# Performance work log

Hardware: AMD Instinct MI355X
Metric: run time of the kernel (lower is better)

The kernel has to match this reference:

```python
import jax, jax.numpy as jnp
import numpy as np

N = 50000   # nodes
E = 800000  # edges (avg degree 16)
H = 4       # heads
IN = 256    # input feature dim
HID = 64    # hidden dim per head (H*HID = 256 = layer-1 indim)
CLS = 40    # num classes


def setup_inputs():
    key = jax.random.key(0)
    ks = jax.random.split(key, 32)
    s = 0.05  # small init scale keeps exp(leaky_relu(...)) numerically tame
    rn = lambda i, shape: jax.random.normal(ks[i], shape, jnp.float32) * s
    inp = {
        'features': jax.random.normal(ks[0], (N, IN), jnp.float32),
        'src': jax.random.randint(ks[1], (E,), 0, N, jnp.int32),
        'dst': jax.random.randint(ks[2], (E,), 0, N, jnp.int32),
        # layer 0 (per-head stacked): fc, attn_l, attn_r
        'W0': rn(3, (H, IN, HID)), 'b0': rn(4, (H, HID)),
        'al0': rn(5, (H, HID)), 'alb0': rn(6, (H,)),
        'ar0': rn(7, (H, HID)), 'arb0': rn(8, (H,)),
        # layer 1 (indim = H*HID = 256), with residual fc per head
        'W1': rn(9, (H, H * HID, HID)), 'b1': rn(10, (H, HID)),
        'al1': rn(11, (H, HID)), 'alb1': rn(12, (H,)),
        'ar1': rn(13, (H, HID)), 'arb1': rn(14, (H,)),
        'R1': rn(15, (H, H * HID, HID)), 'Rb1': rn(16, (H, HID)),
        # final layer (single head, indim = H*HID, outdim = CLS), residual fc
        'Wf': rn(17, (H * HID, CLS)), 'bf': rn(18, (CLS,)),
        'alf': rn(19, (CLS,)), 'alfb': rn(20, (1,)),
        'arf': rn(21, (CLS,)), 'arfb': rn(22, (1,)),
        'Rf': rn(23, (H * HID, CLS)), 'Rbf': rn(24, (CLS,)),
    }
    return inp


def _head(x, W, b, al, alb, ar, arb, src, dst):
    # GATPrepare: ft = Linear(x); a1 = attn_l(ft); a2 = attn_r(ft)
    ft = x @ W + b                              # [N, D]
    a1 = ft @ al + alb                          # [N]
    a2 = ft @ ar + arb                          # [N]
    # edge phase 1: attention = exp(leaky_relu(a2[src] + a1[dst]))
    e = jnp.exp(jax.nn.leaky_relu(a2[src] + a1[dst], 0.01))      # [E]
    # a_sum pass: segment-sum of attention at dst, then normalize (edge softmax)
    denom = jax.ops.segment_sum(e, dst, num_segments=N)          # [N]
    att = (e / denom[dst])[:, None]                              # [E, 1]
    # src_mul_edge + sum: scatter-sum ft[src] * attention into dst
    return jax.ops.segment_sum(ft[src] * att, dst, num_segments=N)  # [N, D]


def reference(features, src, dst,
              W0, b0, al0, alb0, ar0, arb0,
              W1, b1, al1, alb1, ar1, arb1, R1, Rb1,
              Wf, bf, alf, alfb, arf, arfb, Rf, Rbf):
    # layer 0: no residual (hardcoded residual=False for first layer)
    heads = [jax.nn.elu(_head(features, W0[h], b0[h], al0[h], alb0[h], ar0[h], arb0[h], src, dst))
             for h in range(H)]
    x = jnp.concatenate(heads, axis=1)          # [N, H*HID]
    # layer 1: residual via residual_fc (indim != hiddendim)
    heads = [jax.nn.elu(x @ R1[h] + Rb1[h]
                        + _head(x, W1[h], b1[h], al1[h], alb1[h], ar1[h], arb1[h], src, dst))
             for h in range(H)]
    x = jnp.concatenate(heads, axis=1)          # [N, H*HID]
    # final layer: single head to num_classes, residual via residual_fc
    out = jax.nn.elu(x @ Rf + Rbf + _head(x, Wf, bf, alf, alfb, arf, arfb, src, dst))
    return out                                   # [N, CLS]
```

## Files before the change

kernel.cpp:

```cpp
#include <hip/hip_runtime.h>
#include <hip/hip_bf16.h>
#include <math.h>

#define NN   50000
#define NE   800000
#define NHEAD 4
#define HIDD 64
#define DD   256
#define NCLS 40

typedef __attribute__((ext_vector_type(8))) short s8v;
typedef __attribute__((ext_vector_type(4))) float f4v;

static __device__ __forceinline__ float elu_f(float x) {
  return x > 0.f ? x : expm1f(x);
}
static __device__ __forceinline__ float lrelu_exp(float x) {
  float v = x > 0.f ? x : 0.01f * x;
  return expf(v);
}
static __device__ __forceinline__ unsigned short f2bf(float x) {
  union { float f; unsigned u; } v; v.f = x;
  unsigned r = v.u + 0x7fffu + ((v.u >> 16) & 1u);
  return (unsigned short)(r >> 16);
}
static __device__ __forceinline__ float bf2f(unsigned short b) {
  union { unsigned u; float f; } v; v.u = ((unsigned)b) << 16;
  return v.f;
}
static __device__ __forceinline__ float rdlanef(float v, int l) {
  return __uint_as_float(__builtin_amdgcn_readlane(__float_as_uint(v), l));
}

__global__ void pack_w_bf(const float* __restrict__ W,
                          unsigned short* __restrict__ Bh,
                          unsigned short* __restrict__ Bl) {
  int i = blockIdx.x * 256 + threadIdx.x;
  if (i >= 65536) return;
  int n = i >> 8, k = i & 255;
  float v = W[(n >> 6) * (256 * 64) + k * 64 + (n & 63)];
  unsigned short hi = f2bf(v);
  Bh[i] = hi;
  Bl[i] = f2bf(v - bf2f(hi));
}

__global__ void pack_wf_bf(const float* __restrict__ Wf,
                           unsigned short* __restrict__ Bh,
                           unsigned short* __restrict__ Bl) {
  int i = blockIdx.x * 256 + threadIdx.x;
  if (i >= 64 * 256) return;
  int n = i >> 8, k = i & 255;
  float v = (n < NCLS) ? Wf[k * NCLS + n] : 0.f;
  unsigned short hi = f2bf(v);
  Bh[i] = hi;
  Bl[i] = f2bf(v - bf2f(hi));
}

__global__ void split_bf(const float* __restrict__ A,
                         unsigned short* __restrict__ Ah,
                         unsigned short* __restrict__ Al, int n4) {
  int i = blockIdx.x * 256 + threadIdx.x;
  if (i >= n4) return;
  float4 v = ((const float4*)A)[i];
  ushort4 h, l;
  h.x = f2bf(v.x); l.x = f2bf(v.x - bf2f(h.x));
  h.y = f2bf(v.y); l.y = f2bf(v.y - bf2f(h.y));
  h.z = f2bf(v.z); l.z = f2bf(v.z - bf2f(h.z));
  h.w = f2bf(v.w); l.w = f2bf(v.w - bf2f(h.w));
  ((ushort4*)Ah)[i] = h;
  ((ushort4*)Al)[i] = l;
}

template <int BN, int OBF>
__global__ __launch_bounds__(256) void gemm_bf16x3(
    const unsigned short* __restrict__ Ah, const unsigned short* __restrict__ Al,
    const unsigned short* __restrict__ Bth, const unsigned short* __restrict__ Btl,
    const float* __restrict__ bias, float* __restrict__ C,
    unsigned short* __restrict__ Cb,
    int M, int Nc) {
  constexpr int K = 256;
  constexpr int RS = 40;
  constexpr int WM = (BN == 128) ? 2 : 4;
  constexpr int WN = 4 / WM;
  constexpr int MI = (128 / WM) / 16;
  constexpr int NI = (BN / WN) / 16;

  __shared__ unsigned short sAh[128 * RS];
  __shared__ unsigned short sAl[128 * RS];
  __shared__ unsigned short sBh[BN * RS];
  __shared__ unsigned short sBl[BN * RS];

  const int tid = threadIdx.x;
  const int lane = tid & 63;
  const int w = tid >> 6;
  const int wr = w / WN, wc = w % WN;
  const int rowbase = wr * (128 / WM);
  const int colbase = wc * (BN / WN);
  const int row0 = blockIdx.x * 128;
  const int col0 = blockIdx.y * BN;
  const int lm = lane & 15;
  const int lk8 = (lane >> 4) * 8;

  f4v acc[MI][NI];
#pragma unroll
  for (int i = 0; i < MI; i++)
#pragma unroll
    for (int j = 0; j < NI; j++) acc[i][j] = (f4v)(0.f);

  for (int k0 = 0; k0 < K; k0 += 32) {
    __syncthreads();
#pragma unroll
    for (int i = 0; i < 2; ++i) {
      int idx = tid + i * 256;
      int r = idx >> 2, seg = idx & 3;
      int grow = row0 + r;
      s8v hv = (s8v)(short)0, lv = (s8v)(short)0;
      if (grow < M) {
        size_t g = (size_t)grow * K + k0 + seg * 8;
        hv = *(const s8v*)(Ah + g);
        lv = *(const s8v*)(Al + g);
      }
      *(s8v*)&sAh[r * RS + seg * 8] = hv;
      *(s8v*)&sAl[r * RS + seg * 8] = lv;
    }
#pragma unroll
    for (int i = 0; i < BN / 64; ++i) {
      int idx = tid + i * 256;
      int n = idx >> 2, seg = idx & 3;
      size_t g = (size_t)(col0 + n) * K + k0 + seg * 8;
      *(s8v*)&sBh[n * RS + seg * 8] = *(const s8v*)(Bth + g);
      *(s8v*)&sBl[n * RS + seg * 8] = *(const s8v*)(Btl + g);
    }
    __syncthreads();

    s8v ah[MI], al_[MI], bh[NI], bl_[NI];
#pragma unroll
    for (int mi = 0; mi < MI; ++mi) {
      int base = (rowbase + mi * 16 + lm) * RS + lk8;
      ah[mi] = *(const s8v*)&sAh[base];
      al_[mi] = *(const s8v*)&sAl[base];
    }
#pragma unroll
    for (int ni = 0; ni < NI; ++ni) {
      int base = (colbase + ni * 16 + lm) * RS + lk8;
      bh[ni] = *(const s8v*)&sBh[base];
      bl_[ni] = *(const s8v*)&sBl[base];
    }
#pragma unroll
    for (int mi = 0; mi < MI; ++mi)
#pragma unroll
      for (int ni = 0; ni < NI; ++ni)
        acc[mi][ni] = __builtin_amdgcn_mfma_f32_16x16x32_bf16(ah[mi], bh[ni], acc[mi][ni], 0, 0, 0);
#pragma unroll
    for (int mi = 0; mi < MI; ++mi)
#pragma unroll
      for (int ni = 0; ni < NI; ++ni)
        acc[mi][ni] = __builtin_amdgcn_mfma_f32_16x16x32_bf16(ah[mi], bl_[ni], acc[mi][ni], 0, 0, 0);
#pragma unroll
    for (int mi = 0; mi < MI; ++mi)
#pragma unroll
      for (int ni = 0; ni < NI; ++ni)
        acc[mi][ni] = __builtin_amdgcn_mfma_f32_16x16x32_bf16(al_[mi], bh[ni], acc[mi][ni], 0, 0, 0);
  }

#pragma unroll
  for (int ni = 0; ni < NI; ++ni) {
    int col = col0 + colbase + ni * 16 + lm;
    if (col >= Nc) continue;
    float bv = bias[col];
#pragma unroll
    for (int mi = 0; mi < MI; ++mi) {
      int rbase = row0 + rowbase + mi * 16 + (lane >> 4) * 4;
#pragma unroll
      for (int r = 0; r < 4; ++r) {
        int row = rbase + r;
        if (row < M) {
          float o = acc[mi][ni][r] + bv;
          if (OBF) Cb[(size_t)row * Nc + col] = f2bf(o);
          else     C[(size_t)row * Nc + col] = o;
        }
      }
    }
  }
}

__global__ void attn_scores4_bf(const unsigned short* __restrict__ ftb,
                                const float* __restrict__ al, const float* __restrict__ alb,
                                const float* __restrict__ ar, const float* __restrict__ arb,
                                float* __restrict__ a1, float* __restrict__ a2, int n_nodes) {
  int n = blockIdx.x * 4 + (threadIdx.x >> 6);
  if (n >= n_nodes) return;
  int lane = threadIdx.x & 63;
  ushort4 fb = *(const ushort4*)(ftb + (size_t)n * 256 + lane * 4);
  float4 f = make_float4(bf2f(fb.x), bf2f(fb.y), bf2f(fb.z), bf2f(fb.w));
  float4 l4 = *(const float4*)(al + lane * 4);
  float4 r4 = *(const float4*)(ar + lane * 4);
  float p1 = f.x * l4.x + f.y * l4.y + f.z * l4.z + f.w * l4.w;
  float p2 = f.x * r4.x + f.y * r4.y + f.z * r4.z + f.w * r4.w;
#pragma unroll
  for (int m = 1; m < 16; m <<= 1) {
    p1 += __shfl_xor(p1, m);
    p2 += __shfl_xor(p2, m);
  }
  if ((lane & 15) == 0) {
    int h = lane >> 4;
    a1[n * 4 + h] = p1 + alb[h];
    a2[n * 4 + h] = p2 + arb[h];
  }
}

__global__ void attn_scores1(const float* __restrict__ ftf,
                             const float* __restrict__ alf, const float* __restrict__ alfb,
                             const float* __restrict__ arf, const float* __restrict__ arfb,
                             float* __restrict__ a1, float* __restrict__ a2, int n_nodes) {
  int n = blockIdx.x * 4 + (threadIdx.x >> 6);
  if (n >= n_nodes) return;
  int lane = threadIdx.x & 63;
  float v = (lane < NCLS) ? ftf[(size_t)n * NCLS + lane] : 0.f;
  float p1 = (lane < NCLS) ? v * alf[lane] : 0.f;
  float p2 = (lane < NCLS) ? v * arf[lane] : 0.f;
#pragma unroll
  for (int m = 1; m < 64; m <<= 1) {
    p1 += __shfl_xor(p1, m);
    p2 += __shfl_xor(p2, m);
  }
  if (lane == 0) {
    a1[n] = p1 + alfb[0];
    a2[n] = p2 + arfb[0];
  }
}

__global__ void count_deg(const int* __restrict__ dst, int* __restrict__ deg) {
  int e = blockIdx.x * blockDim.x + threadIdx.x;
  if (e < NE) atomicAdd(&deg[dst[e]], 1);
}

__global__ void scan_deg(const int* __restrict__ deg, int* __restrict__ row_ptr, int n) {
  __shared__ int partials[1024];
  int t = threadIdx.x;
  int chunk = (n + 1023) >> 10;
  int base = t * chunk;
  int lim = min(base + chunk, n);
  int sum = 0;
  for (int i = base; i < lim; ++i) sum += deg[i];
  partials[t] = sum;
  __syncthreads();
  for (int off = 1; off < 1024; off <<= 1) {
    int v = (t >= off) ? partials[t - off] : 0;
    __syncthreads();
    partials[t] += v;
    __syncthreads();
  }
  int run = (t == 0) ? 0 : partials[t - 1];
  if (t == 0) row_ptr[0] = 0;
  for (int i = base; i < lim; ++i) {
    run += deg[i];
    row_ptr[i + 1] = run;
  }
}

__global__ void copy_int(const int* __restrict__ a, int* __restrict__ b, int n) {
  int i = blockIdx.x * blockDim.x + threadIdx.x;
  if (i < n) b[i] = a[i];
}

__global__ void scatter_e(const int* __restrict__ dst, int* __restrict__ cursor,
                          int* __restrict__ eidx) {
  int e = blockIdx.x * blockDim.x + threadIdx.x;
  if (e >= NE) return;
  int d = dst[e];
  int pos = atomicAdd(&cursor[d], 1);
  eidx[pos] = e;
}

__global__ __launch_bounds__(256) void gather_wave4(
    const unsigned short* __restrict__ ftb, const float* __restrict__ a1,
    const float* __restrict__ a2, const float* __restrict__ res,
    const int* __restrict__ row_ptr, const int* __restrict__ eidx,
    const int* __restrict__ src,
    unsigned short* __restrict__ outh, unsigned short* __restrict__ outl) {
  const int n = blockIdx.x * 4 + (threadIdx.x >> 6);
  if (n >= NN) return;
  const int lane = threadIdx.x & 63;
  const int c = lane >> 4;
  const int b = row_ptr[n], en = row_ptr[n + 1];
  const int deg = en - b;
  const float4 a1v = *(const float4*)(a1 + (size_t)n * 4);
  float4 accv = make_float4(0.f, 0.f, 0.f, 0.f);
  float den = 0.f;

  for (int cb = 0; cb < deg; cb += 64) {
    int cnt = min(64, deg - cb);
    int s = 0;
    float4 wv = make_float4(0.f, 0.f, 0.f, 0.f);
    if (lane < cnt) {
      s = src[eidx[b + cb + lane]];
      float4 as_ = *(const float4*)(a2 + (size_t)s * 4);
      wv.x = lrelu_exp(as_.x + a1v.x);
      wv.y = lrelu_exp(as_.y + a1v.y);
      wv.z = lrelu_exp(as_.z + a1v.z);
      wv.w = lrelu_exp(as_.w + a1v.w);
    }
    int i = 0;
    for (; i + 4 <= cnt; i += 4) {
      int s0 = __builtin_amdgcn_readlane(s, i + 0);
      int s1 = __builtin_amdgcn_readlane(s, i + 1);
      int s2 = __builtin_amdgcn_readlane(s, i + 2);
      int s3 = __builtin_amdgcn_readlane(s, i + 3);
      ushort4 f0 = *(const ushort4*)(ftb + (size_t)s0 * DD + lane * 4);
      ushort4 f1 = *(const ushort4*)(ftb + (size_t)s1 * DD + lane * 4);
      ushort4 f2 = *(const ushort4*)(ftb + (size_t)s2 * DD + lane * 4);
      ushort4 f3 = *(const ushort4*)(ftb + (size_t)s3 * DD + lane * 4);
      float x0 = rdlanef(wv.x, i + 0), y0 = rdlanef(wv.y, i + 0),
            z0 = rdlanef(wv.z, i + 0), u0 = rdlanef(wv.w, i + 0);
      float x1 = rdlanef(wv.x, i + 1), y1 = rdlanef(wv.y, i + 1),
            z1 = rdlanef(wv.z, i + 1), u1 = rdlanef(wv.w, i + 1);
      float x2 = rdlanef(wv.x, i + 2), y2 = rdlanef(wv.y, i + 2),
            z2 = rdlanef(wv.z, i + 2), u2 = rdlanef(wv.w, i + 2);
      float x3 = rdlanef(wv.x, i + 3), y3 = rdlanef(wv.y, i + 3),
            z3 = rdlanef(wv.z, i + 3), u3 = rdlanef(wv.w, i + 3);
      float w0 = (c == 0) ? x0 : (c == 1) ? y0 : (c == 2) ? z0 : u0;
      float w1 = (c == 0) ? x1 : (c == 1) ? y1 : (c == 2) ? z1 : u1;
      float w2 = (c == 0) ? x2 : (c == 1) ? y2 : (c == 2) ? z2 : u2;
      float w3 = (c == 0) ? x3 : (c == 1) ? y3 : (c == 2) ? z3 : u3;
      accv.x = fmaf(bf2f(f0.x), w0, accv.x);
      accv.y = fmaf(bf2f(f0.y), w0, accv.y);
      accv.z = fmaf(bf2f(f0.z), w0, accv.z);
      accv.w = fmaf(bf2f(f0.w), w0, accv.w);
      accv.x = fmaf(bf2f(f1.x), w1, accv.x);
      accv.y = fmaf(bf2f(f1.y), w1, accv.y);
      accv.z = fmaf(bf2f(f1.z), w1, accv.z);
      accv.w = fmaf(bf2f(f1.w), w1, accv.w);
      accv.x = fmaf(bf2f(f2.x), w2, accv.x);
      accv.y = fmaf(bf2f(f2.y), w2, accv.y);
      accv.z = fmaf(bf2f(f2.z), w2, accv.z);
      accv.w = fmaf(bf2f(f2.w), w2, accv.w);
      accv.x = fmaf(bf2f(f3.x), w3, accv.x);
      accv.y = fmaf(bf2f(f3.y), w3, accv.y);
      accv.z = fmaf(bf2f(f3.z), w3, accv.z);
      accv.w = fmaf(bf2f(f3.w), w3, accv.w);
      den += (w0 + w1) + (w2 + w3);
    }
    for (; i < cnt; ++i) {
      int si = __builtin_amdgcn_readlane(s, i);
      float fx = rdlanef(wv.x, i), fy = rdlanef(wv.y, i),
            fz = rdlanef(wv.z, i), fw = rdlanef(wv.w, i);
      float wc = (c == 0) ? fx : (c == 1) ? fy : (c == 2) ? fz : fw;
      ushort4 fv = *(const ushort4*)(ftb + (size_t)si * DD + lane * 4);
      accv.x = fmaf(bf2f(fv.x), wc, accv.x);
      accv.y = fmaf(bf2f(fv.y), wc, accv.y);
      accv.z = fmaf(bf2f(fv.z), wc, accv.z);
      accv.w = fmaf(bf2f(fv.w), wc, accv.w);
      den += wc;
    }
  }
  float invden = (deg > 0) ? 1.f / den : 0.f;
  float4 r = (res != nullptr) ? *(const float4*)(res + (size_t)n * DD + lane * 4)
                              : make_float4(0.f, 0.f, 0.f, 0.f);
  float4 o;
  o.x = elu_f(r.x + accv.x * invden);
  o.y = elu_f(r.y + accv.y * invden);
  o.z = elu_f(r.z + accv.z * invden);
  o.w = elu_f(r.w + accv.w * invden);
  ushort4 h, l;
  h.x = f2bf(o.x); l.x = f2bf(o.x - bf2f(h.x));
  h.y = f2bf(o.y); l.y = f2bf(o.y - bf2f(h.y));
  h.z = f2bf(o.z); l.z = f2bf(o.z - bf2f(h.z));
  h.w = f2bf(o.w); l.w = f2bf(o.w - bf2f(h.w));
  *(ushort4*)(outh + (size_t)n * DD + lane * 4) = h;
  *(ushort4*)(outl + (size_t)n * DD + lane * 4) = l;
}

__global__ __launch_bounds__(64) void gather_fused1(
    const float* __restrict__ ft, const float* __restrict__ a1,
    const float* __restrict__ a2, const float* __restrict__ res,
    const int* __restrict__ row_ptr, const int* __restrict__ eidx,
    const int* __restrict__ src, float* __restrict__ out) {
  const int n = blockIdx.x;
  const int d = threadIdx.x;
  const int b = row_ptr[n], en = row_ptr[n + 1];
  const int deg = en - b;
  const float a1n = a1[n];
  float acc = 0.f;
  float den = 0.f;

  for (int cb = 0; cb < deg; cb += 64) {
    int cnt = min(64, deg - cb);
    int s = 0;
    float wv = 0.f;
    if (d < cnt) {
      s = src[eidx[b + cb + d]];
      wv = lrelu_exp(a2[s] + a1n);
    }
    int i = 0;
    for (; i + 4 <= cnt; i += 4) {
      int s0 = __builtin_amdgcn_readlane(s, i + 0);
      int s1 = __builtin_amdgcn_readlane(s, i + 1);
      int s2 = __builtin_amdgcn_readlane(s, i + 2);
      int s3 = __builtin_amdgcn_readlane(s, i + 3);
      float w0 = rdlanef(wv, i + 0), w1 = rdlanef(wv, i + 1);
      float w2 = rdlanef(wv, i + 2), w3 = rdlanef(wv, i + 3);
      if (d < NCLS) {
        float v0 = ft[(size_t)s0 * NCLS + d];
        float v1 = ft[(size_t)s1 * NCLS + d];
        float v2 = ft[(size_t)s2 * NCLS + d];
        float v3 = ft[(size_t)s3 * NCLS + d];
        acc = fmaf(v0, w0, acc);
        acc = fmaf(v1, w1, acc);
        acc = fmaf(v2, w2, acc);
        acc = fmaf(v3, w3, acc);
      }
      den += (w0 + w1) + (w2 + w3);
    }
    for (; i < cnt; ++i) {
      int si = __builtin_amdgcn_readlane(s, i);
      float wi = rdlanef(wv, i);
      if (d < NCLS) acc = fmaf(ft[(size_t)si * NCLS + d], wi, acc);
      den += wi;
    }
  }
  float invden = (deg > 0) ? 1.f / den : 0.f;
  if (d < NCLS) {
    float r = res[(size_t)n * NCLS + d];
    out[(size_t)n * NCLS + d] = elu_f(r + acc * invden);
  }
}

extern "C" void kernel_launch(void* const* d_in, const int* in_sizes, int n_in,
                              void* d_out, int out_size, void* d_ws, size_t ws_size,
                              hipStream_t stream) {
  const float* features = (const float*)d_in[0];
  const int* src = (const int*)d_in[1];
  const int* dst = (const int*)d_in[2];
  const float* W0 = (const float*)d_in[3];
  const float* b0 = (const float*)d_in[4];
  const float* al0 = (const float*)d_in[5];
  const float* alb0 = (const float*)d_in[6];
  const float* ar0 = (const float*)d_in[7];
  const float* arb0 = (const float*)d_in[8];
  const float* W1 = (const float*)d_in[9];
  const float* b1 = (const float*)d_in[10];
  const float* al1 = (const float*)d_in[11];
  const float* alb1 = (const float*)d_in[12];
  const float* ar1 = (const float*)d_in[13];
  const float* arb1 = (const float*)d_in[14];
  const float* R1 = (const float*)d_in[15];
  const float* Rb1 = (const float*)d_in[16];
  const float* Wf = (const float*)d_in[17];
  const float* bfc = (const float*)d_in[18];
  const float* alf = (const float*)d_in[19];
  const float* alfb = (const float*)d_in[20];
  const float* arf = (const float*)d_in[21];
  const float* arfb = (const float*)d_in[22];
  const float* Rf = (const float*)d_in[23];
  const float* Rbf = (const float*)d_in[24];
  float* out = (float*)d_out;

  float* p = (float*)d_ws;
  float* B1 = p;  p += (size_t)NN * 256;
  float* B2 = p;  p += (size_t)NN * 256;
  float* B3 = p;  p += (size_t)NN * 256;
  float* a1 = p;  p += (size_t)NN * 4;
  float* a2 = p;  p += (size_t)NN * 4;
  unsigned short* us = (unsigned short*)p;
  unsigned short* Wp0h = us; us += 65536;
  unsigned short* Wp0l = us; us += 65536;
  unsigned short* Wp1h = us; us += 65536;
  unsigned short* Wp1l = us; us += 65536;
  unsigned short* Rp1h = us; us += 65536;
  unsigned short* Rp1l = us; us += 65536;
  unsigned short* Wfh = us;  us += 64 * 256;
  unsigned short* Wfl = us;  us += 64 * 256;
  unsigned short* Rfh = us;  us += 64 * 256;
  unsigned short* Rfl = us;  us += 64 * 256;
  unsigned short* Ah = us;   us += (size_t)NN * 256;
  unsigned short* Al = us;   us += (size_t)NN * 256;
  unsigned short* ftb = us;  us += (size_t)NN * 256;
  int* ip = (int*)us;
  int* row_ptr = ip; ip += NN + 1;
  int* cursor = ip;  ip += NN;
  int* deg = ip;     ip += NN;
  int* eidx = ip;    ip += NE;

  const int EB = (NE + 255) / 256;
  const int N4 = NN * 64;

  pack_w_bf<<<256, 256, 0, stream>>>(W0, Wp0h, Wp0l);
  pack_w_bf<<<256, 256, 0, stream>>>(W1, Wp1h, Wp1l);
  pack_w_bf<<<256, 256, 0, stream>>>(R1, Rp1h, Rp1l);
  pack_wf_bf<<<64, 256, 0, stream>>>(Wf, Wfh, Wfl);
  pack_wf_bf<<<64, 256, 0, stream>>>(Rf, Rfh, Rfl);

  hipMemsetAsync(deg, 0, NN * sizeof(int), stream);
  count_deg<<<EB, 256, 0, stream>>>(dst, deg);
  scan_deg<<<1, 1024, 0, stream>>>(deg, row_ptr, NN);
  copy_int<<<(NN + 255) / 256, 256, 0, stream>>>(row_ptr, cursor, NN);
  scatter_e<<<EB, 256, 0, stream>>>(dst, cursor, eidx);

  const int MB = (NN + 127) / 128;
  dim3 gbig(MB, 2);
  dim3 gsm(MB, 1);
  const int GW = (NN + 3) / 4;

  split_bf<<<(N4 + 255) / 256, 256, 0, stream>>>(features, Ah, Al, N4);
  gemm_bf16x3<128, 1><<<gbig, 256, 0, stream>>>(Ah, Al, Wp0h, Wp0l, b0, nullptr, ftb, NN, 256);
  attn_scores4_bf<<<(NN + 3) / 4, 256, 0, stream>>>(ftb, al0, alb0, ar0, arb0, a1, a2, NN);
  gather_wave4<<<GW, 256, 0, stream>>>(ftb, a1, a2, nullptr, row_ptr, eidx, src, Ah, Al);

  gemm_bf16x3<128, 1><<<gbig, 256, 0, stream>>>(Ah, Al, Wp1h, Wp1l, b1, nullptr, ftb, NN, 256);
  gemm_bf16x3<128, 0><<<gbig, 256, 0, stream>>>(Ah, Al, Rp1h, Rp1l, Rb1, B3, nullptr, NN, 256);
  attn_scores4_bf<<<(NN + 3) / 4, 256, 0, stream>>>(ftb, al1, alb1, ar1, arb1, a1, a2, NN);
  gather_wave4<<<GW, 256, 0, stream>>>(ftb, a1, a2, B3, row_ptr, eidx, src, Ah, Al);

  gemm_bf16x3<64, 0><<<gsm, 256, 0, stream>>>(Ah, Al, Wfh, Wfl, bfc, B1, nullptr, NN, NCLS);
  gemm_bf16x3<64, 0><<<gsm, 256, 0, stream>>>(Ah, Al, Rfh, Rfl, Rbf, B2, nullptr, NN, NCLS);
  attn_scores1<<<(NN + 3) / 4, 256, 0, stream>>>(B1, alf, alfb, arf, arfb, a1, a2, NN);
  gather_fused1<<<NN, 64, 0, stream>>>(B1, a1, a2, B2, row_ptr, eidx, src, out);
}
```

Baseline: 734.5 us.

## Merge weight-pack launches, fold cursor init into scan, deepen gather unroll with LDS weights

Five weight-packing launches become one kernel that picks its source by block index. The scan kernel now writes the cursor array directly, which removes the copy_int launch. The 256-wide gather stores per-edge attention weights in shared memory and reads the lane's head weight from there, replacing sixteen readlanes plus select chains per four edges. Both gather kernels unroll eight edges per iteration to keep more loads in flight. The trade-offs are extra register pressure, shared-memory use, and a manual lgkmcnt wait that relies on the whole wave staying in lockstep, since no barrier is used.

```diff
diff --git a/kernel.cpp b/kernel.cpp
--- a/kernel.cpp
+++ b/kernel.cpp
@@ -32,25 +32,26 @@
   return __uint_as_float(__builtin_amdgcn_readlane(__float_as_uint(v), l));
 }
 
-__global__ void pack_w_bf(const float* __restrict__ W,
-                          unsigned short* __restrict__ Bh,
-                          unsigned short* __restrict__ Bl) {
-  int i = blockIdx.x * 256 + threadIdx.x;
-  if (i >= 65536) return;
+__global__ void pack_all(const float* __restrict__ W0, const float* __restrict__ W1,
+                         const float* __restrict__ R1, const float* __restrict__ Wf,
+                         const float* __restrict__ Rf,
+                         unsigned short* __restrict__ Wp0h, unsigned short* __restrict__ Wp0l,
+                         unsigned short* __restrict__ Wp1h, unsigned short* __restrict__ Wp1l,
+                         unsigned short* __restrict__ Rp1h, unsigned short* __restrict__ Rp1l,
+                         unsigned short* __restrict__ Wfh, unsigned short* __restrict__ Wfl,
+                         unsigned short* __restrict__ Rfh, unsigned short* __restrict__ Rfl) {
+  int bid = blockIdx.x;
+  const float* S; unsigned short *Bh, *Bl; int big;
+  if (bid < 256)      { S = W0; Bh = Wp0h; Bl = Wp0l; big = 1; }
+  else if (bid < 512) { S = W1; Bh = Wp1h; Bl = Wp1l; big = 1; bid -= 256; }
+  else if (bid < 768) { S = R1; Bh = Rp1h; Bl = Rp1l; big = 1; bid -= 512; }
+  else if (bid < 832) { S = Wf; Bh = Wfh;  Bl = Wfl;  big = 0; bid -= 768; }
+  else                { S = Rf; Bh = Rfh;  Bl = Rfl;  big = 0; bid -= 832; }
+  int i = bid * 256 + threadIdx.x;
   int n = i >> 8, k = i & 255;
-  float v = W[(n >> 6) * (256 * 64) + k * 64 + (n & 63)];
-  unsigned short hi = f2bf(v);
-  Bh[i] = hi;
-  Bl[i] = f2bf(v - bf2f(hi));
-}
-
-__global__ void pack_wf_bf(const float* __restrict__ Wf,
-                           unsigned short* __restrict__ Bh,
-                           unsigned short* __restrict__ Bl) {
-  int i = blockIdx.x * 256 + threadIdx.x;
-  if (i >= 64 * 256) return;
-  int n = i >> 8, k = i & 255;
-  float v = (n < NCLS) ? Wf[k * NCLS + n] : 0.f;
+  float v;
+  if (big) v = S[(n >> 6) * (256 * 64) + k * 64 + (n & 63)];
+  else     v = (n < NCLS) ? S[k * NCLS + n] : 0.f;
   unsigned short hi = f2bf(v);
   Bh[i] = hi;
   Bl[i] = f2bf(v - bf2f(hi));
@@ -235,7 +236,8 @@
   if (e < NE) atomicAdd(&deg[dst[e]], 1);
 }
 
-__global__ void scan_deg(const int* __restrict__ deg, int* __restrict__ row_ptr, int n) {
+__global__ void scan_deg(const int* __restrict__ deg, int* __restrict__ row_ptr,
+                         int* __restrict__ cursor, int n) {
   __shared__ int partials[1024];
   int t = threadIdx.x;
   int chunk = (n + 1023) >> 10;
@@ -254,14 +256,10 @@
   int run = (t == 0) ? 0 : partials[t - 1];
   if (t == 0) row_ptr[0] = 0;
   for (int i = base; i < lim; ++i) {
+    cursor[i] = run;
     run += deg[i];
     row_ptr[i + 1] = run;
   }
-}
-
-__global__ void copy_int(const int* __restrict__ a, int* __restrict__ b, int n) {
-  int i = blockIdx.x * blockDim.x + threadIdx.x;
-  if (i < n) b[i] = a[i];
 }
 
 __global__ void scatter_e(const int* __restrict__ dst, int* __restrict__ cursor,
@@ -279,10 +277,12 @@
     const int* __restrict__ row_ptr, const int* __restrict__ eidx,
     const int* __restrict__ src,
     unsigned short* __restrict__ outh, unsigned short* __restrict__ outl) {
-  const int n = blockIdx.x * 4 + (threadIdx.x >> 6);
+  __shared__ float s_w[4][64][4];
+  const int wid = threadIdx.x >> 6;
+  const int n = blockIdx.x * 4 + wid;
   if (n >= NN) return;
   const int lane = threadIdx.x & 63;
-  const int c = lane >> 4;
+  const int h = lane >> 4;
   const int b = row_ptr[n], en = row_ptr[n + 1];
   const int deg = en - b;
   const float4 a1v = *(const float4*)(a1 + (size_t)n * 4);
@@ -292,37 +292,43 @@
   for (int cb = 0; cb < deg; cb += 64) {
     int cnt = min(64, deg - cb);
     int s = 0;
-    float4 wv = make_float4(0.f, 0.f, 0.f, 0.f);
     if (lane < cnt) {
       s = src[eidx[b + cb + lane]];
       float4 as_ = *(const float4*)(a2 + (size_t)s * 4);
-      wv.x = lrelu_exp(as_.x + a1v.x);
-      wv.y = lrelu_exp(as_.y + a1v.y);
-      wv.z = lrelu_exp(as_.z + a1v.z);
-      wv.w = lrelu_exp(as_.w + a1v.w);
-    }
+      float4 w4;
+      w4.x = lrelu_exp(as_.x + a1v.x);
+      w4.y = lrelu_exp(as_.y + a1v.y);
+      w4.z = lrelu_exp(as_.z + a1v.z);
+      w4.w = lrelu_exp(as_.w + a1v.w);
+      *(float4*)&s_w[wid][lane][0] = w4;
+    }
+    asm volatile("s_waitcnt lgkmcnt(0)" ::: "memory");
     int i = 0;
-    for (; i + 4 <= cnt; i += 4) {
+    for (; i + 8 <= cnt; i += 8) {
       int s0 = __builtin_amdgcn_readlane(s, i + 0);
       int s1 = __builtin_amdgcn_readlane(s, i + 1);
       int s2 = __builtin_amdgcn_readlane(s, i + 2);
       int s3 = __builtin_amdgcn_readlane(s, i + 3);
+      int s4 = __builtin_amdgcn_readlane(s, i + 4);
+      int s5 = __builtin_amdgcn_readlane(s, i + 5);
+      int s6 = __builtin_amdgcn_readlane(s, i + 6);
+      int s7 = __builtin_amdgcn_readlane(s, i + 7);
+      float w0 = s_w[wid][i + 0][h];
+      float w1 = s_w[wid][i + 1][h];
+      float w2 = s_w[wid][i + 2][h];
+      float w3 = s_w[wid][i + 3][h];
+      float w4_ = s_w[wid][i + 4][h];
+      float w5 = s_w[wid][i + 5][h];
+      float w6 = s_w[wid][i + 6][h];
+      float w7 = s_w[wid][i + 7][h];
       ushort4 f0 = *(const ushort4*)(ftb + (size_t)s0 * DD + lane * 4);
       ushort4 f1 = *(const ushort4*)(ftb + (size_t)s1 * DD + lane * 4);
       ushort4 f2 = *(const ushort4*)(ftb + (size_t)s2 * DD + lane * 4);
       ushort4 f3 = *(const ushort4*)(ftb + (size_t)s3 * DD + lane * 4);
-      float x0 = rdlanef(wv.x, i + 0), y0 = rdlanef(wv.y, i + 0),
-            z0 = rdlanef(wv.z, i + 0), u0 = rdlanef(wv.w, i + 0);
-      float x1 = rdlanef(wv.x, i + 1), y1 = rdlanef(wv.y, i + 1),
-            z1 = rdlanef(wv.z, i + 1), u1 = rdlanef(wv.w, i + 1);
-      float x2 = rdlanef(wv.x, i + 2), y2 = rdlanef(wv.y, i + 2),
-            z2 = rdlanef(wv.z, i + 2), u2 = rdlanef(wv.w, i + 2);
-      float x3 = rdlanef(wv.x, i + 3), y3 = rdlanef(wv.y, i + 3),
-            z3 = rdlanef(wv.z, i + 3), u3 = rdlanef(wv.w, i + 3);
-      float w0 = (c == 0) ? x0 : (c == 1) ? y0 : (c == 2) ? z0 : u0;
-      float w1 = (c == 0) ? x1 : (c == 1) ? y1 : (c == 2) ? z1 : u1;
-      float w2 = (c == 0) ? x2 : (c == 1) ? y2 : (c == 2) ? z2 : u2;
-      float w3 = (c == 0) ? x3 : (c == 1) ? y3 : (c == 2) ? z3 : u3;
+      ushort4 f4 = *(const ushort4*)(ftb + (size_t)s4 * DD + lane * 4);
+      ushort4 f5 = *(const ushort4*)(ftb + (size_t)s5 * DD + lane * 4);
+      ushort4 f6 = *(const ushort4*)(ftb + (size_t)s6 * DD + lane * 4);
+      ushort4 f7 = *(const ushort4*)(ftb + (size_t)s7 * DD + lane * 4);
       accv.x = fmaf(bf2f(f0.x), w0, accv.x);
       accv.y = fmaf(bf2f(f0.y), w0, accv.y);
       accv.z = fmaf(bf2f(f0.z), w0, accv.z);
@@ -339,19 +345,33 @@
       accv.y = fmaf(bf2f(f3.y), w3, accv.y);
       accv.z = fmaf(bf2f(f3.z), w3, accv.z);
       accv.w = fmaf(bf2f(f3.w), w3, accv.w);
-      den += (w0 + w1) + (w2 + w3);
+      accv.x = fmaf(bf2f(f4.x), w4_, accv.x);
+      accv.y = fmaf(bf2f(f4.y), w4_, accv.y);
+      accv.z = fmaf(bf2f(f4.z), w4_, accv.z);
+      accv.w = fmaf(bf2f(f4.w), w4_, accv.w);
+      accv.x = fmaf(bf2f(f5.x), w5, accv.x);
+      accv.y = fmaf(bf2f(f5.y), w5, accv.y);
+      accv.z = fmaf(bf2f(f5.z), w5, accv.z);
+      accv.w = fmaf(bf2f(f5.w), w5, accv.w);
+      accv.x = fmaf(bf2f(f6.x), w6, accv.x);
+      accv.y = fmaf(bf2f(f6.y), w6, accv.y);
+      accv.z = fmaf(bf2f(f6.z), w6, accv.z);
+      accv.w = fmaf(bf2f(f6.w), w6, accv.w);
+      accv.x = fmaf(bf2f(f7.x), w7, accv.x);
+      accv.y = fmaf(bf2f(f7.y), w7, accv.y);
+      accv.z = fmaf(bf2f(f7.z), w7, accv.z);
+      accv.w = fmaf(bf2f(f7.w), w7, accv.w);
+      den += ((w0 + w1) + (w2 + w3)) + ((w4_ + w5) + (w6 + w7));
     }
     for (; i < cnt; ++i) {
       int si = __builtin_amdgcn_readlane(s, i);
-      float fx = rdlanef(wv.x, i), fy = rdlanef(wv.y, i),
-            fz = rdlanef(wv.z, i), fw = rdlanef(wv.w, i);
-      float wc = (c == 0) ? fx : (c == 1) ? fy : (c == 2) ? fz : fw;
+      float wi = s_w[wid][i][h];
       ushort4 fv = *(const ushort4*)(ftb + (size_t)si * DD + lane * 4);
-      accv.x = fmaf(bf2f(fv.x), wc, accv.x);
-      accv.y = fmaf(bf2f(fv.y), wc, accv.y);
-      accv.z = fmaf(bf2f(fv.z), wc, accv.z);
-      accv.w = fmaf(bf2f(fv.w), wc, accv.w);
-      den += wc;
+      accv.x = fmaf(bf2f(fv.x), wi, accv.x);
+      accv.y = fmaf(bf2f(fv.y), wi, accv.y);
+      accv.z = fmaf(bf2f(fv.z), wi, accv.z);
+      accv.w = fmaf(bf2f(fv.w), wi, accv.w);
+      den += wi;
     }
   }
   float invden = (deg > 0) ? 1.f / den : 0.f;
@@ -362,13 +382,13 @@
   o.y = elu_f(r.y + accv.y * invden);
   o.z = elu_f(r.z + accv.z * invden);
   o.w = elu_f(r.w + accv.w * invden);
-  ushort4 h, l;
-  h.x = f2bf(o.x); l.x = f2bf(o.x - bf2f(h.x));
-  h.y = f2bf(o.y); l.y = f2bf(o.y - bf2f(h.y));
-  h.z = f2bf(o.z); l.z = f2bf(o.z - bf2f(h.z));
-  h.w = f2bf(o.w); l.w = f2bf(o.w - bf2f(h.w));
-  *(ushort4*)(outh + (size_t)n * DD + lane * 4) = h;
-  *(ushort4*)(outl + (size_t)n * DD + lane * 4) = l;
+  ushort4 hh, ll;
+  hh.x = f2bf(o.x); ll.x = f2bf(o.x - bf2f(hh.x));
+  hh.y = f2bf(o.y); ll.y = f2bf(o.y - bf2f(hh.y));
+  hh.z = f2bf(o.z); ll.z = f2bf(o.z - bf2f(hh.z));
+  hh.w = f2bf(o.w); ll.w = f2bf(o.w - bf2f(hh.w));
+  *(ushort4*)(outh + (size_t)n * DD + lane * 4) = hh;
+  *(ushort4*)(outl + (size_t)n * DD + lane * 4) = ll;
 }
 
 __global__ __launch_bounds__(64) void gather_fused1(
@@ -393,24 +413,38 @@
       wv = lrelu_exp(a2[s] + a1n);
     }
     int i = 0;
-    for (; i + 4 <= cnt; i += 4) {
+    for (; i + 8 <= cnt; i += 8) {
       int s0 = __builtin_amdgcn_readlane(s, i + 0);
       int s1 = __builtin_amdgcn_readlane(s, i + 1);
       int s2 = __builtin_amdgcn_readlane(s, i + 2);
       int s3 = __builtin_amdgcn_readlane(s, i + 3);
+      int s4 = __builtin_amdgcn_readlane(s, i + 4);
+      int s5 = __builtin_amdgcn_readlane(s, i + 5);
+      int s6 = __builtin_amdgcn_readlane(s, i + 6);
+      int s7 = __builtin_amdgcn_readlane(s, i + 7);
       float w0 = rdlanef(wv, i + 0), w1 = rdlanef(wv, i + 1);
       float w2 = rdlanef(wv, i + 2), w3 = rdlanef(wv, i + 3);
+      float w4_ = rdlanef(wv, i + 4), w5 = rdlanef(wv, i + 5);
+      float w6 = rdlanef(wv, i + 6), w7 = rdlanef(wv, i + 7);
       if (d < NCLS) {
         float v0 = ft[(size_t)s0 * NCLS + d];
         float v1 = ft[(size_t)s1 * NCLS + d];
         float v2 = ft[(size_t)s2 * NCLS + d];
         float v3 = ft[(size_t)s3 * NCLS + d];
+        float v4 = ft[(size_t)s4 * NCLS + d];
+        float v5 = ft[(size_t)s5 * NCLS + d];
+        float v6 = ft[(size_t)s6 * NCLS + d];
+        float v7 = ft[(size_t)s7 * NCLS + d];
         acc = fmaf(v0, w0, acc);
         acc = fmaf(v1, w1, acc);
         acc = fmaf(v2, w2, acc);
         acc = fmaf(v3, w3, acc);
+        acc = fmaf(v4, w4_, acc);
+        acc = fmaf(v5, w5, acc);
+        acc = fmaf(v6, w6, acc);
+        acc = fmaf(v7, w7, acc);
       }
-      den += (w0 + w1) + (w2 + w3);
+      den += ((w0 + w1) + (w2 + w3)) + ((w4_ + w5) + (w6 + w7));
     }
     for (; i < cnt; ++i) {
       int si = __builtin_amdgcn_readlane(s, i);
@@ -485,16 +519,13 @@
   const int EB = (NE + 255) / 256;
   const int N4 = NN * 64;
 
-  pack_w_bf<<<256, 256, 0, stream>>>(W0, Wp0h, Wp0l);
-  pack_w_bf<<<256, 256, 0, stream>>>(W1, Wp1h, Wp1l);
-  pack_w_bf<<<256, 256, 0, stream>>>(R1, Rp1h, Rp1l);
-  pack_wf_bf<<<64, 256, 0, stream>>>(Wf, Wfh, Wfl);
-  pack_wf_bf<<<64, 256, 0, stream>>>(Rf, Rfh, Rfl);
+  pack_all<<<896, 256, 0, stream>>>(W0, W1, R1, Wf, Rf,
+                                    Wp0h, Wp0l, Wp1h, Wp1l, Rp1h, Rp1l,
+                                    Wfh, Wfl, Rfh, Rfl);
 
   hipMemsetAsync(deg, 0, NN * sizeof(int), stream);
   count_deg<<<EB, 256, 0, stream>>>(dst, deg);
-  scan_deg<<<1, 1024, 0, stream>>>(deg, row_ptr, NN);
-  copy_int<<<(NN + 255) / 256, 256, 0, stream>>>(row_ptr, cursor, NN);
+  scan_deg<<<1, 1024, 0, stream>>>(deg, row_ptr, cursor, NN);
   scatter_e<<<EB, 256, 0, stream>>>(dst, cursor, eidx);
 
   const int MB = (NN + 127) / 128;
```

Result: no change. 746.5 us (+1.6%).
